# Kernel tuning notes

Measured on AMD Instinct MI355X. Metric: run time of the kernel, lower is better.

## Reference

```python
import jax, jax.numpy as jnp
import numpy as np

V, D, L, H, S, B = 50257, 768, 12, 12, 1024, 2
DH = D // H          # 64
F4 = 4 * D           # 3072
EPS = 1e-5


def _ln(x, g, b):
    m = jnp.mean(x, axis=-1, keepdims=True)
    v = jnp.mean((x - m) ** 2, axis=-1, keepdims=True)
    return (x - m) * jax.lax.rsqrt(v + EPS) * g + b


def setup_inputs() -> dict:
    key = jax.random.key(0)
    ks = jax.random.split(key, 16)
    n = lambda k, shape: jax.random.normal(k, shape, jnp.float32) * 0.02
    return {
        "tokens": jax.random.randint(ks[0], (B, S), 0, V),
        "tok_emb": n(ks[1], (V, D)),
        "pos_emb": n(ks[2], (S, D)),
        "ln1_g": jnp.ones((L, D), jnp.float32), "ln1_b": jnp.zeros((L, D), jnp.float32),
        "wq": n(ks[3], (L, D, D)), "bq": jnp.zeros((L, D), jnp.float32),
        "wk": n(ks[4], (L, D, D)), "bk": jnp.zeros((L, D), jnp.float32),
        "wv": n(ks[5], (L, D, D)), "bv": jnp.zeros((L, D), jnp.float32),
        "wo": n(ks[6], (L, D, D)), "bo": jnp.zeros((L, D), jnp.float32),
        "ln2_g": jnp.ones((L, D), jnp.float32), "ln2_b": jnp.zeros((L, D), jnp.float32),
        "w1": n(ks[7], (L, D, F4)), "b1": jnp.zeros((L, F4), jnp.float32),
        "w2": n(ks[8], (L, F4, D)), "b2": jnp.zeros((L, D), jnp.float32),
        "fn_g": jnp.ones((D,), jnp.float32), "fn_b": jnp.zeros((D,), jnp.float32),
        "head_w": n(ks[9], (D, V)), "head_b": jnp.zeros((V,), jnp.float32),
    }


def reference(tokens, tok_emb, pos_emb, ln1_g, ln1_b, wq, bq, wk, bk, wv, bv,
              wo, bo, ln2_g, ln2_b, w1, b1, w2, b2, fn_g, fn_b, head_w, head_b):
    b_, s_ = tokens.shape
    x = tok_emb[tokens] + pos_emb[:s_]                       # [B,S,D]
    causal = jnp.tril(jnp.ones((s_, s_), bool))              # allow j <= i
    scale = 1.0 / np.sqrt(DH)

    def block(x, p):
        g1, c1, Wq, Bq, Wk, Bk, Wv, Bv_, Wo, Bo, g2, c2, W1, B1, W2, B2 = p
        h = _ln(x, g1, c1)
        q = (h @ Wq + Bq).reshape(b_, s_, H, DH)
        k = (h @ Wk + Bk).reshape(b_, s_, H, DH)
        v = (h @ Wv + Bv_).reshape(b_, s_, H, DH)
        scores = jnp.einsum('bqhd,bkhd->bhqk', q, k) * scale  # [B,H,S,S]
        scores = jnp.where(causal, scores, -jnp.inf)
        attn = jax.nn.softmax(scores, axis=-1)
        o = jnp.einsum('bhqk,bkhd->bqhd', attn, v).reshape(b_, s_, D)
        x = x + (o @ Wo + Bo)
        h2 = _ln(x, g2, c2)
        ff = jax.nn.gelu(h2 @ W1 + B1, approximate=False) @ W2 + B2
        return x + ff, None

    x, _ = jax.lax.scan(block, x, (ln1_g, ln1_b, wq, bq, wk, bk, wv, bv,
                                   wo, bo, ln2_g, ln2_b, w1, b1, w2, b2))
    return _ln(x, fn_g, fn_b) @ head_w + head_b               # [B,S,V]
```

## Files before the change

### kernel.cpp

```cpp
#include <hip/hip_runtime.h>

typedef __bf16 bf16;
typedef bf16 bf16x8 __attribute__((ext_vector_type(8)));
typedef float f32x4 __attribute__((ext_vector_type(4)));

#define SQ  1024
#define DIM 768
#define NH  12
#define NL  12
#define F4  3072
#define NPADV 50304
#define NVOC  50257

__device__ __forceinline__ void async16(bf16* lds, const bf16* g) {
  __builtin_amdgcn_global_load_lds(
      (const __attribute__((address_space(1))) unsigned int*)g,
      (__attribute__((address_space(3))) unsigned int*)lds, 16, 0, 0);
}

__global__ __launch_bounds__(256) void embed_kernel(
    const int* __restrict__ tokens, const float* __restrict__ tok_emb,
    const float* __restrict__ pos_emb, float* __restrict__ x) {
  int row = blockIdx.x;
  int s   = row & (SQ - 1);
  int tok = tokens[row];
  for (int i = threadIdx.x; i < DIM; i += 256)
    x[(size_t)row * DIM + i] = tok_emb[(size_t)tok * DIM + i] + pos_emb[(size_t)s * DIM + i];
}

__global__ __launch_bounds__(256) void ln_kernel(
    const float* __restrict__ x, const float* __restrict__ g,
    const float* __restrict__ b, bf16* __restrict__ out) {
  int row = blockIdx.x;
  const float* xr = x + (size_t)row * DIM;
  int t = threadIdx.x;
  float v0 = xr[t], v1 = xr[t + 256], v2 = xr[t + 512];
  float s  = v0 + v1 + v2;
  float sq = v0 * v0 + v1 * v1 + v2 * v2;
#pragma unroll
  for (int off = 32; off; off >>= 1) {
    s  += __shfl_xor(s, off);
    sq += __shfl_xor(sq, off);
  }
  __shared__ float rs[4], rq[4];
  int wid = t >> 6, lane = t & 63;
  if (lane == 0) { rs[wid] = s; rq[wid] = sq; }
  __syncthreads();
  float S = rs[0] + rs[1] + rs[2] + rs[3];
  float Q = rq[0] + rq[1] + rq[2] + rq[3];
  float mean = S * (1.0f / DIM);
  float var  = Q * (1.0f / DIM) - mean * mean;
  float rstd = rsqrtf(var + 1e-5f);
  bf16* orow = out + (size_t)row * DIM;
  orow[t]       = (bf16)((v0 - mean) * rstd * g[t]       + b[t]);
  orow[t + 256] = (bf16)((v1 - mean) * rstd * g[t + 256] + b[t + 256]);
  orow[t + 512] = (bf16)((v2 - mean) * rstd * g[t + 512] + b[t + 512]);
}

__global__ __launch_bounds__(256) void tconv_kernel(
    const float* __restrict__ src, bf16* __restrict__ dst,
    int K, int N, size_t s_stride, size_t d_stride) {
  __shared__ float tile[32][33];
  const float* s = src + blockIdx.z * s_stride;
  bf16* d = dst + blockIdx.z * d_stride;
  int n0 = blockIdx.x * 32, k0 = blockIdx.y * 32;
  int tx = threadIdx.x & 31, ty = threadIdx.x >> 5;
#pragma unroll
  for (int r = 0; r < 32; r += 8) {
    int n = n0 + tx;
    tile[ty + r][tx] = (n < N) ? s[(size_t)(k0 + ty + r) * N + n] : 0.f;
  }
  __syncthreads();
#pragma unroll
  for (int r = 0; r < 32; r += 8)
    d[(size_t)(n0 + ty + r) * K + k0 + tx] = (bf16)tile[tx][ty + r];
}

__global__ __launch_bounds__(256) void packb_kernel(
    const float* __restrict__ bq, const float* __restrict__ bk,
    const float* __restrict__ bv, float* __restrict__ qkvb) {
  int l = blockIdx.x, t = threadIdx.x;
  for (int i = t; i < DIM; i += 256) {
    qkvb[(size_t)l * 2304 + i]        = bq[(size_t)l * DIM + i];
    qkvb[(size_t)l * 2304 + 768 + i]  = bk[(size_t)l * DIM + i];
    qkvb[(size_t)l * 2304 + 1536 + i] = bv[(size_t)l * DIM + i];
  }
}

template <int BM, int DEPTH, bool GELU_, bool RESID, bool OUTBF, bool NT>
__global__ __launch_bounds__(BM == 128 ? 512 : 256) void gemm_bt(
    const bf16* __restrict__ A, const bf16* __restrict__ BT,
    const float* __restrict__ bias, const float* __restrict__ resid,
    float* __restrict__ outF, bf16* __restrict__ outB,
    int M, int N, int K) {
  constexpr int BK = 64;
  constexpr int WAVES = (BM == 128) ? 8 : 4;
  constexpr int BROW = 128 / WAVES;
  constexpr int NB = BROW / 8;
  constexpr int EPLD = 68;
  constexpr size_t GBYTES = (size_t)DEPTH * (BM + 128) * BK * 2;
  constexpr size_t EBYTES = NT ? (size_t)WAVES * 32 * EPLD * 4 : 0;
  constexpr size_t SBYTES = (EBYTES > GBYTES) ? EBYTES : GBYTES;
  __shared__ __align__(16) char smem[SBYTES];

  const int gx = gridDim.x;
  const int lid = blockIdx.y * gx + blockIdx.x;
  const int q8 = (gx * gridDim.y) >> 3;
  const int work = (lid & 7) * q8 + (lid >> 3);
  const int m0 = (work % gx) * BM, n0 = (work / gx) * 128;

  const int t = threadIdx.x, w = t >> 6, lane = t & 63;
  const int wm = (w >> 1) * 32, wn = (w & 1) * 64;
  const int row16 = lane & 15, kg = lane >> 4;
  const int srow = lane >> 3;
  const int scol = ((lane & 7) ^ srow) * 8;
  f32x4 acc[2][4] = {};

  const bf16* Abase = A  + (size_t)(m0 + w * 16 + srow) * K + scol;
  const bf16* Bbase = BT + (size_t)(n0 + w * BROW + srow) * K + scol;

  auto stage = [&](int buf, int k0) {
    bf16* as = (bf16*)smem + (size_t)buf * BM * BK;
    bf16* bs = (bf16*)smem + (size_t)DEPTH * BM * BK + (size_t)buf * 128 * BK;
#pragma unroll
    for (int i = 0; i < 2; i++)
      async16(as + (w * 16 + i * 8) * BK, Abase + (size_t)(i * 8) * K + k0);
#pragma unroll
    for (int i = 0; i < NB; i++)
      async16(bs + (w * BROW + i * 8) * BK, Bbase + (size_t)(i * 8) * K + k0);
  };

  const int nk = K / BK;
  stage(0, 0);
  if constexpr (DEPTH == 3) stage(1, BK);
  for (int ki = 0; ki < nk; ki++) {
    const int cur = ki % DEPTH;
    const bf16* Ac = (const bf16*)smem + (size_t)cur * BM * BK;
    const bf16* Bc = (const bf16*)smem + (size_t)DEPTH * BM * BK + (size_t)cur * 128 * BK;
    if (ki + DEPTH - 1 < nk) {
      stage((ki + DEPTH - 1) % DEPTH, (ki + DEPTH - 1) * BK);
      if constexpr (DEPTH == 3)      asm volatile("s_waitcnt vmcnt(12)" ::: "memory");
      else if constexpr (BM == 128)  asm volatile("s_waitcnt vmcnt(4)"  ::: "memory");
      else                           asm volatile("s_waitcnt vmcnt(6)"  ::: "memory");
    } else if (DEPTH == 3 && ki + 1 < nk) {
      asm volatile("s_waitcnt vmcnt(6)" ::: "memory");
    } else {
      asm volatile("s_waitcnt vmcnt(0)" ::: "memory");
    }
    __builtin_amdgcn_s_barrier();
    __builtin_amdgcn_sched_barrier(0);
    const int psw = row16 & 7;
#pragma unroll
    for (int kk = 0; kk < 2; kk++) {
      const int pc = ((kk * 4 + kg) ^ psw) * 8;
      bf16x8 af[2], bfv[4];
#pragma unroll
      for (int i = 0; i < 2; i++)
        af[i] = *(const bf16x8*)(&Ac[(wm + i * 16 + row16) * BK + pc]);
#pragma unroll
      for (int j = 0; j < 4; j++)
        bfv[j] = *(const bf16x8*)(&Bc[(wn + j * 16 + row16) * BK + pc]);
#pragma unroll
      for (int i = 0; i < 2; i++)
#pragma unroll
        for (int j = 0; j < 4; j++)
          acc[i][j] = __builtin_amdgcn_mfma_f32_16x16x32_bf16(af[i], bfv[j], acc[i][j], 0, 0, 0);
    }
    if (ki + 1 < nk) {
      __builtin_amdgcn_s_barrier();
      __builtin_amdgcn_sched_barrier(0);
    }
  }

  if constexpr (NT) {
    __syncthreads();
    float* ws = (float*)smem + (size_t)w * 32 * EPLD;
#pragma unroll
    for (int i = 0; i < 2; i++)
#pragma unroll
      for (int j = 0; j < 4; j++) {
        int col = n0 + wn + j * 16 + row16;
        float bi = (col < N) ? bias[col] : 0.f;
#pragma unroll
        for (int r = 0; r < 4; r++)
          ws[(i * 16 + kg * 4 + r) * EPLD + j * 16 + row16] = acc[i][j][r] + bi;
      }
    const int lr = lane >> 4, lc = (lane & 15) * 4;
#pragma unroll
    for (int p = 0; p < 8; p++) {
      int row = m0 + (w >> 1) * 32 + p * 4 + lr;
      int col = n0 + (w & 1) * 64 + lc;
      f32x4 v = *(const f32x4*)&ws[(p * 4 + lr) * EPLD + lc];
      float* dst = outF + (size_t)row * N + col;
      if (col + 3 < N) {
        __builtin_nontemporal_store(v, (f32x4*)dst);
      } else {
#pragma unroll
        for (int e = 0; e < 4; e++)
          if (col + e < N) __builtin_nontemporal_store(v[e], dst + e);
      }
    }
  } else {
#pragma unroll
    for (int i = 0; i < 2; i++)
#pragma unroll
      for (int j = 0; j < 4; j++) {
        int col = n0 + wn + j * 16 + row16;
        if (col < N) {
          float bi = bias[col];
#pragma unroll
          for (int r = 0; r < 4; r++) {
            int row = m0 + wm + i * 16 + kg * 4 + r;
            float val = acc[i][j][r] + bi;
            if constexpr (GELU_) val = 0.5f * val * (1.0f + erff(val * 0.70710678f));
            if constexpr (RESID) val += resid[(size_t)row * N + col];
            if constexpr (OUTBF) outB[(size_t)row * N + col] = (bf16)val;
            else                 outF[(size_t)row * N + col] = val;
          }
        }
      }
  }
}

__global__ __launch_bounds__(512) void fattn_kernel(
    const bf16* __restrict__ qkv, bf16* __restrict__ o) {
  constexpr int LP  = 72;
  constexpr int LPV = 136;
  constexpr int LPP = 136;
  constexpr int LDQ = 2304;
  __shared__ bf16 Ks[128 * LP];
  __shared__ bf16 Vt[64 * LPV];
  __shared__ bf16 Ps[8][16 * LPP];

  const int qt = 7 - (blockIdx.x & 7);
  const int hb = blockIdx.x >> 3;
  const int h  = hb % NH;
  const int b  = hb / NH;
  const int t = threadIdx.x;
  const int w = t >> 6, lane = t & 63;
  const int row16 = lane & 15, kg = lane >> 4;

  const bf16* kbase = qkv + 768  + (size_t)(b * SQ) * LDQ + h * 64;
  const bf16* vbase = qkv + 1536 + (size_t)(b * SQ) * LDQ + h * 64;

  const int wq0  = qt * 128 + w * 16;
  const int qrow = wq0 + row16;
  const bf16* qptr = qkv + (size_t)(b * SQ + qrow) * LDQ + h * 64;
  const bf16x8 qf0 = *(const bf16x8*)(qptr + kg * 8);
  const bf16x8 qf1 = *(const bf16x8*)(qptr + 32 + kg * 8);

  f32x4 oacc[4] = {};
  float mrow[4] = {-1e30f, -1e30f, -1e30f, -1e30f};
  float lrow[4] = {0.f, 0.f, 0.f, 0.f};
  const int myq = wq0 + kg * 4;
  const int ntiles = qt + 1;

  for (int jb0 = 0; jb0 < ntiles; jb0++) {
    const int j0 = jb0 * 128;
    __syncthreads();
#pragma unroll
    for (int it = 0; it < 2; it++) {
      int idx = t + it * 512;
      int key = idx >> 3, d8 = (idx & 7) * 8;
      *(uint4*)(&Ks[key * LP + d8]) =
          *(const uint4*)(kbase + (size_t)(j0 + key) * LDQ + d8);
      bf16x8 vv = *(const bf16x8*)(vbase + (size_t)(j0 + key) * LDQ + d8);
      int kc = key >> 3, kl = key & 7;
#pragma unroll
      for (int e = 0; e < 8; e++) {
        int d = d8 + e;
        Vt[d * LPV + ((kc ^ (d >> 3)) << 3) + kl] = vv[e];
      }
    }
    __syncthreads();

    f32x4 sacc[8];
    __builtin_amdgcn_s_setprio(1);
#pragma unroll
    for (int jb = 0; jb < 8; jb++) {
      bf16x8 kf0 = *(const bf16x8*)(&Ks[(jb * 16 + row16) * LP + kg * 8]);
      bf16x8 kf1 = *(const bf16x8*)(&Ks[(jb * 16 + row16) * LP + 32 + kg * 8]);
      f32x4 sa = {};
      sa = __builtin_amdgcn_mfma_f32_16x16x32_bf16(qf0, kf0, sa, 0, 0, 0);
      sa = __builtin_amdgcn_mfma_f32_16x16x32_bf16(qf1, kf1, sa, 0, 0, 0);
      sacc[jb] = sa;
    }
    __builtin_amdgcn_s_setprio(0);

    constexpr float SC = 0.125f * 1.44269504f;
    if (j0 + 127 > wq0) {
#pragma unroll
      for (int jb = 0; jb < 8; jb++) {
        int keyg = j0 + jb * 16 + row16;
#pragma unroll
        for (int r = 0; r < 4; r++)
          sacc[jb][r] = (keyg <= myq + r) ? sacc[jb][r] * SC : -1e30f;
      }
    } else {
#pragma unroll
      for (int jb = 0; jb < 8; jb++)
#pragma unroll
        for (int r = 0; r < 4; r++)
          sacc[jb][r] *= SC;
    }

    float p[8][4];
#pragma unroll
    for (int r = 0; r < 4; r++) {
      float mx = sacc[0][r];
#pragma unroll
      for (int jb = 1; jb < 8; jb++) mx = fmaxf(mx, sacc[jb][r]);
      mx = fmaxf(mx, __shfl_xor(mx, 1));
      mx = fmaxf(mx, __shfl_xor(mx, 2));
      mx = fmaxf(mx, __shfl_xor(mx, 4));
      mx = fmaxf(mx, __shfl_xor(mx, 8));
      float mn = fmaxf(mrow[r], mx);
      float al = exp2f(mrow[r] - mn);
      mrow[r] = mn;
      float ls = 0.f;
#pragma unroll
      for (int jb = 0; jb < 8; jb++) {
        float pv = exp2f(sacc[jb][r] - mn);
        p[jb][r] = pv;
        ls += pv;
      }
      ls += __shfl_xor(ls, 1);
      ls += __shfl_xor(ls, 2);
      ls += __shfl_xor(ls, 4);
      ls += __shfl_xor(ls, 8);
      lrow[r] = lrow[r] * al + ls;
#pragma unroll
      for (int dt = 0; dt < 4; dt++) oacc[dt][r] *= al;
    }

    bf16* pw = &Ps[w][0];
#pragma unroll
    for (int jb = 0; jb < 8; jb++)
#pragma unroll
      for (int r = 0; r < 4; r++)
        pw[(kg * 4 + r) * LPP + jb * 16 + row16] = (bf16)p[jb][r];

    bf16x8 pf[4];
#pragma unroll
    for (int m = 0; m < 4; m++)
      pf[m] = *(const bf16x8*)(&pw[row16 * LPP + m * 32 + kg * 8]);

    __builtin_amdgcn_s_setprio(1);
#pragma unroll
    for (int dt = 0; dt < 4; dt++) {
      int drow = dt * 16 + row16;
      int sw = drow >> 3;
#pragma unroll
      for (int m = 0; m < 4; m++) {
        bf16x8 vf = *(const bf16x8*)(&Vt[drow * LPV + (((m * 4 + kg) ^ sw) << 3)]);
        oacc[dt] = __builtin_amdgcn_mfma_f32_16x16x32_bf16(pf[m], vf, oacc[dt], 0, 0, 0);
      }
    }
    __builtin_amdgcn_s_setprio(0);
  }

  bf16* obase = o + (size_t)(b * SQ + wq0 + kg * 4) * DIM + h * 64;
#pragma unroll
  for (int r = 0; r < 4; r++) {
    float inv = 1.0f / lrow[r];
#pragma unroll
    for (int dt = 0; dt < 4; dt++)
      obase[(size_t)r * DIM + dt * 16 + row16] = (bf16)(oacc[dt][r] * inv);
  }
}

template <bool GELU_, bool RESID, bool OUTBF>
__global__ __launch_bounds__(256) void gemm_kernel(
    const bf16* __restrict__ A, const float* __restrict__ W,
    const float* __restrict__ bias, const float* __restrict__ resid,
    float* __restrict__ outF, bf16* __restrict__ outB,
    int M, int N, int K) {
  constexpr int BM = 128, BN = 128, BK = 32, LDP = 40;
  __shared__ bf16 As[BM * LDP];
  __shared__ bf16 Bs[BN * LDP];
  int m0 = blockIdx.y * BM;
  int n0 = blockIdx.x * BN;
  int t = threadIdx.x;
  int wid = t >> 6, lane = t & 63;
  int wm = (wid >> 1) * 64, wn = (wid & 1) * 64;
  int row16 = lane & 15, kg = lane >> 4;
  f32x4 acc[4][4] = {};
  bool edge = (n0 + BN > N);

  for (int k0 = 0; k0 < K; k0 += BK) {
#pragma unroll
    for (int r2 = 0; r2 < 2; r2++) {
      int idx = t + r2 * 256;
      int row = idx >> 2, c8 = (idx & 3) * 8;
      uint4 va = *reinterpret_cast<const uint4*>(A + (size_t)(m0 + row) * K + k0 + c8);
      *reinterpret_cast<uint4*>(&As[row * LDP + c8]) = va;
    }
#pragma unroll
    for (int r = 0; r < 8; r++) {
      int idx = t + r * 256;
      int n = idx & 127, kp = idx >> 7;
      int kk = kp * 2;
      float w0 = 0.f, w1 = 0.f;
      if (!edge || (n0 + n) < N) {
        w0 = W[(size_t)(k0 + kk) * N + n0 + n];
        w1 = W[(size_t)(k0 + kk + 1) * N + n0 + n];
      }
      bf16 b0 = (bf16)w0, b1 = (bf16)w1;
      union { bf16 b[2]; unsigned int u; } pk;
      pk.b[0] = b0; pk.b[1] = b1;
      *reinterpret_cast<unsigned int*>(&Bs[n * LDP + kk]) = pk.u;
    }
    __syncthreads();
    bf16x8 af[4], bfv[4];
#pragma unroll
    for (int i = 0; i < 4; i++)
      af[i] = *reinterpret_cast<const bf16x8*>(&As[(wm + i * 16 + row16) * LDP + kg * 8]);
#pragma unroll
    for (int j = 0; j < 4; j++)
      bfv[j] = *reinterpret_cast<const bf16x8*>(&Bs[(wn + j * 16 + row16) * LDP + kg * 8]);
#pragma unroll
    for (int i = 0; i < 4; i++)
#pragma unroll
      for (int j = 0; j < 4; j++)
        acc[i][j] = __builtin_amdgcn_mfma_f32_16x16x32_bf16(af[i], bfv[j], acc[i][j], 0, 0, 0);
    __syncthreads();
  }

  int crow = (lane >> 4) * 4;
  int ccol = lane & 15;
#pragma unroll
  for (int i = 0; i < 4; i++)
#pragma unroll
    for (int j = 0; j < 4; j++) {
      int col = n0 + wn + j * 16 + ccol;
      if (col < N) {
        float bi = bias[col];
#pragma unroll
        for (int r = 0; r < 4; r++) {
          int row = m0 + wm + i * 16 + crow + r;
          float val = acc[i][j][r] + bi;
          if constexpr (GELU_) val = 0.5f * val * (1.0f + erff(val * 0.70710678f));
          if constexpr (RESID) val += resid[(size_t)row * N + col];
          if constexpr (OUTBF) outB[(size_t)row * N + col] = (bf16)val;
          else                 outF[(size_t)row * N + col] = val;
        }
      }
    }
}

__global__ __launch_bounds__(256) void fattn_legacy_kernel(
    const bf16* __restrict__ q, const bf16* __restrict__ k,
    const bf16* __restrict__ v, bf16* __restrict__ o) {
  constexpr int LP = 72;
  __shared__ bf16 Ks[64 * LP];
  __shared__ bf16 Vt[64 * LP];
  __shared__ bf16 Ps[4][16 * LP];
  const int qt = blockIdx.x & 15;
  const int h  = (blockIdx.x >> 4) % NH;
  const int b  = blockIdx.x / (16 * NH);
  const int t = threadIdx.x;
  const int w = t >> 6, lane = t & 63;
  const int row16 = lane & 15, kg = lane >> 4;
  const bf16* kbase = k + (size_t)(b * SQ) * DIM + h * 64;
  const bf16* vbase = v + (size_t)(b * SQ) * DIM + h * 64;
  const int qrow = qt * 64 + w * 16 + row16;
  const bf16* qptr = q + (size_t)(b * SQ + qrow) * DIM + h * 64;
  const bf16x8 qf0 = *(const bf16x8*)(qptr + kg * 8);
  const bf16x8 qf1 = *(const bf16x8*)(qptr + 32 + kg * 8);
  f32x4 oacc[4] = {};
  float mrow[4] = {-1e30f, -1e30f, -1e30f, -1e30f};
  float lrow[4] = {0.f, 0.f, 0.f, 0.f};
  const int myq = qt * 64 + w * 16 + kg * 4;
  for (int jb0 = 0; jb0 <= qt; jb0++) {
    const int j0 = jb0 * 64;
    __syncthreads();
#pragma unroll
    for (int it = 0; it < 2; it++) {
      int idx = t + it * 256;
      int key = idx >> 3, d8 = (idx & 7) * 8;
      *(uint4*)(&Ks[key * LP + d8]) = *(const uint4*)(kbase + (size_t)(j0 + key) * DIM + d8);
    }
#pragma unroll
    for (int it = 0; it < 2; it++) {
      int idx = t + it * 256;
      int key = idx >> 3, d8 = (idx & 7) * 8;
      bf16x8 vv = *(const bf16x8*)(vbase + (size_t)(j0 + key) * DIM + d8);
      int kc = key >> 3, kl = key & 7;
#pragma unroll
      for (int e = 0; e < 8; e++) {
        int d = d8 + e;
        Vt[d * LP + ((kc ^ (d >> 3)) << 3) + kl] = vv[e];
      }
    }
    __syncthreads();
    f32x4 sacc[4];
#pragma unroll
    for (int jb = 0; jb < 4; jb++) {
      bf16x8 kf0 = *(const bf16x8*)(&Ks[(jb * 16 + row16) * LP + kg * 8]);
      bf16x8 kf1 = *(const bf16x8*)(&Ks[(jb * 16 + row16) * LP + 32 + kg * 8]);
      f32x4 sa = {};
      sa = __builtin_amdgcn_mfma_f32_16x16x32_bf16(qf0, kf0, sa, 0, 0, 0);
      sa = __builtin_amdgcn_mfma_f32_16x16x32_bf16(qf1, kf1, sa, 0, 0, 0);
      sacc[jb] = sa;
    }
    constexpr float SC = 0.125f * 1.44269504f;
    if (jb0 == qt) {
#pragma unroll
      for (int jb = 0; jb < 4; jb++) {
        int keyg = j0 + jb * 16 + row16;
#pragma unroll
        for (int r = 0; r < 4; r++)
          sacc[jb][r] = (keyg <= myq + r) ? sacc[jb][r] * SC : -1e30f;
      }
    } else {
#pragma unroll
      for (int jb = 0; jb < 4; jb++)
#pragma unroll
        for (int r = 0; r < 4; r++)
          sacc[jb][r] *= SC;
    }
    float p[4][4];
#pragma unroll
    for (int r = 0; r < 4; r++) {
      float mx = fmaxf(fmaxf(sacc[0][r], sacc[1][r]), fmaxf(sacc[2][r], sacc[3][r]));
      mx = fmaxf(mx, __shfl_xor(mx, 1));
      mx = fmaxf(mx, __shfl_xor(mx, 2));
      mx = fmaxf(mx, __shfl_xor(mx, 4));
      mx = fmaxf(mx, __shfl_xor(mx, 8));
      float mn = fmaxf(mrow[r], mx);
      float al = exp2f(mrow[r] - mn);
      mrow[r] = mn;
      float ls = 0.f;
#pragma unroll
      for (int jb = 0; jb < 4; jb++) {
        float pv = exp2f(sacc[jb][r] - mn);
        p[jb][r] = pv;
        ls += pv;
      }
      ls += __shfl_xor(ls, 1);
      ls += __shfl_xor(ls, 2);
      ls += __shfl_xor(ls, 4);
      ls += __shfl_xor(ls, 8);
      lrow[r] = lrow[r] * al + ls;
#pragma unroll
      for (int dt = 0; dt < 4; dt++) oacc[dt][r] *= al;
    }
    bf16* pw = &Ps[w][0];
#pragma unroll
    for (int jb = 0; jb < 4; jb++)
#pragma unroll
      for (int r = 0; r < 4; r++)
        pw[(kg * 4 + r) * LP + jb * 16 + row16] = (bf16)p[jb][r];
    bf16x8 pf0 = *(const bf16x8*)(&pw[row16 * LP + kg * 8]);
    bf16x8 pf1 = *(const bf16x8*)(&pw[row16 * LP + 32 + kg * 8]);
#pragma unroll
    for (int dt = 0; dt < 4; dt++) {
      int drow = dt * 16 + row16;
      int sw = (drow >> 3) & 7;
      bf16x8 vf0 = *(const bf16x8*)(&Vt[drow * LP + ((kg ^ sw) << 3)]);
      bf16x8 vf1 = *(const bf16x8*)(&Vt[drow * LP + (((4 + kg) ^ sw) << 3)]);
      oacc[dt] = __builtin_amdgcn_mfma_f32_16x16x32_bf16(pf0, vf0, oacc[dt], 0, 0, 0);
      oacc[dt] = __builtin_amdgcn_mfma_f32_16x16x32_bf16(pf1, vf1, oacc[dt], 0, 0, 0);
    }
  }
  bf16* obase = o + (size_t)(b * SQ + qt * 64 + w * 16 + kg * 4) * DIM + h * 64;
#pragma unroll
  for (int r = 0; r < 4; r++) {
    float inv = 1.0f / lrow[r];
#pragma unroll
    for (int dt = 0; dt < 4; dt++)
      obase[(size_t)r * DIM + dt * 16 + row16] = (bf16)(oacc[dt][r] * inv);
  }
}

extern "C" void kernel_launch(void* const* d_in, const int* in_sizes, int n_in,
                              void* d_out, int out_size, void* d_ws, size_t ws_size,
                              hipStream_t stream) {
  const int*   tokens  = (const int*)  d_in[0];
  const float* tok_emb = (const float*)d_in[1];
  const float* pos_emb = (const float*)d_in[2];
  const float* ln1_g   = (const float*)d_in[3];
  const float* ln1_b   = (const float*)d_in[4];
  const float* wq      = (const float*)d_in[5];
  const float* bq      = (const float*)d_in[6];
  const float* wk      = (const float*)d_in[7];
  const float* bk      = (const float*)d_in[8];
  const float* wv      = (const float*)d_in[9];
  const float* bv      = (const float*)d_in[10];
  const float* wo      = (const float*)d_in[11];
  const float* bo      = (const float*)d_in[12];
  const float* ln2_g   = (const float*)d_in[13];
  const float* ln2_b   = (const float*)d_in[14];
  const float* w1      = (const float*)d_in[15];
  const float* b1      = (const float*)d_in[16];
  const float* w2      = (const float*)d_in[17];
  const float* b2      = (const float*)d_in[18];
  const float* fn_g    = (const float*)d_in[19];
  const float* fn_b    = (const float*)d_in[20];
  const float* head_w  = (const float*)d_in[21];
  const float* head_b  = (const float*)d_in[22];
  float* out = (float*)d_out;

  const int ROWS = 2 * SQ;
  char* p = (char*)d_ws;
  float* x   = (float*)p;  p += (size_t)ROWS * DIM * 4;
  bf16*  h   = (bf16*)p;   p += (size_t)ROWS * DIM * 2;
  bf16*  qkv = (bf16*)p;   p += (size_t)ROWS * 2304 * 2;
  bf16*  ao  = (bf16*)p;   p += (size_t)ROWS * DIM * 2;
  bf16*  mid = (bf16*)p;   p += (size_t)ROWS * F4  * 2;
  bf16*  WqkvT = (bf16*)p; p += (size_t)NL * 2304 * DIM * 2;
  bf16*  WoT   = (bf16*)p; p += (size_t)NL * DIM * DIM * 2;
  bf16*  W1T   = (bf16*)p; p += (size_t)NL * F4 * DIM * 2;
  bf16*  W2T   = (bf16*)p; p += (size_t)NL * DIM * F4 * 2;
  bf16*  WhT   = (bf16*)p; p += (size_t)NPADV * DIM * 2;
  float* qkvb  = (float*)p; p += (size_t)NL * 2304 * 4;
  size_t need = (size_t)(p - (char*)d_ws);

  embed_kernel<<<ROWS, 256, 0, stream>>>(tokens, tok_emb, pos_emb, x);

  if (ws_size >= need) {
    {
      dim3 gdd(DIM / 32, DIM / 32, NL);
      size_t ss = (size_t)DIM * DIM, ds = (size_t)2304 * DIM;
      tconv_kernel<<<gdd, 256, 0, stream>>>(wq, WqkvT,                       DIM, DIM, ss, ds);
      tconv_kernel<<<gdd, 256, 0, stream>>>(wk, WqkvT + (size_t)768  * DIM,  DIM, DIM, ss, ds);
      tconv_kernel<<<gdd, 256, 0, stream>>>(wv, WqkvT + (size_t)1536 * DIM,  DIM, DIM, ss, ds);
      tconv_kernel<<<gdd, 256, 0, stream>>>(wo, WoT, DIM, DIM, ss, ss);
      dim3 g1(F4 / 32, DIM / 32, NL);
      tconv_kernel<<<g1, 256, 0, stream>>>(w1, W1T, DIM, F4, (size_t)DIM * F4, (size_t)F4 * DIM);
      dim3 g2(DIM / 32, F4 / 32, NL);
      tconv_kernel<<<g2, 256, 0, stream>>>(w2, W2T, F4, DIM, (size_t)F4 * DIM, (size_t)DIM * F4);
      dim3 gh(NPADV / 32, DIM / 32, 1);
      tconv_kernel<<<gh, 256, 0, stream>>>(head_w, WhT, DIM, NVOC, 0, 0);
      packb_kernel<<<NL, 256, 0, stream>>>(bq, bk, bv, qkvb);
    }

    dim3 gQKV(32, 2304 / 128);
    dim3 gD(32, DIM / 128);
    dim3 gF(32, F4 / 128);
    dim3 gV(16, NPADV / 128);

    for (int l = 0; l < NL; l++) {
      ln_kernel<<<ROWS, 256, 0, stream>>>(x, ln1_g + l * DIM, ln1_b + l * DIM, h);
      gemm_bt<64, 2, false, false, true, false><<<gQKV, 256, 0, stream>>>(
          h, WqkvT + (size_t)l * 2304 * DIM, qkvb + (size_t)l * 2304,
          nullptr, nullptr, qkv, ROWS, 2304, DIM);
      fattn_kernel<<<2 * NH * (SQ / 128), 512, 0, stream>>>(qkv, ao);
      gemm_bt<64, 3, false, true, false, false><<<gD, 256, 0, stream>>>(
          ao, WoT + (size_t)l * DIM * DIM, bo + l * DIM, x, x, nullptr, ROWS, DIM, DIM);
      ln_kernel<<<ROWS, 256, 0, stream>>>(x, ln2_g + l * DIM, ln2_b + l * DIM, h);
      gemm_bt<64, 2, true, false, true, false><<<gF, 256, 0, stream>>>(
          h, W1T + (size_t)l * F4 * DIM, b1 + l * F4, nullptr, nullptr, mid, ROWS, F4, DIM);
      gemm_bt<64, 3, false, true, false, false><<<gD, 256, 0, stream>>>(
          mid, W2T + (size_t)l * DIM * F4, b2 + l * DIM, x, x, nullptr, ROWS, DIM, F4);
    }
    ln_kernel<<<ROWS, 256, 0, stream>>>(x, fn_g, fn_b, h);
    gemm_bt<128, 2, false, false, false, true><<<gV, 512, 0, stream>>>(
        h, WhT, head_b, nullptr, out, nullptr, ROWS, NVOC, DIM);
  } else {
    char* q2 = (char*)d_ws;
    float* xf  = (float*)q2; q2 += (size_t)ROWS * DIM * 4;
    bf16*  hf  = (bf16*)q2;  q2 += (size_t)ROWS * DIM * 2;
    bf16*  qb2 = (bf16*)q2;  q2 += (size_t)ROWS * DIM * 2;
    bf16*  kb2 = (bf16*)q2;  q2 += (size_t)ROWS * DIM * 2;
    bf16*  vb2 = (bf16*)q2;  q2 += (size_t)ROWS * DIM * 2;
    bf16*  ao2 = (bf16*)q2;  q2 += (size_t)ROWS * DIM * 2;
    bf16*  mi2 = (bf16*)q2;  q2 += (size_t)ROWS * F4  * 2;
    dim3 gD(DIM / 128, ROWS / 128);
    dim3 gF(F4 / 128, ROWS / 128);
    dim3 gV((NVOC + 127) / 128, ROWS / 128);
    for (int l = 0; l < NL; l++) {
      size_t wo_off = (size_t)l * DIM * DIM;
      ln_kernel<<<ROWS, 256, 0, stream>>>(xf, ln1_g + l * DIM, ln1_b + l * DIM, hf);
      gemm_kernel<false, false, true><<<gD, 256, 0, stream>>>(
          hf, wq + wo_off, bq + l * DIM, nullptr, nullptr, qb2, ROWS, DIM, DIM);
      gemm_kernel<false, false, true><<<gD, 256, 0, stream>>>(
          hf, wk + wo_off, bk + l * DIM, nullptr, nullptr, kb2, ROWS, DIM, DIM);
      gemm_kernel<false, false, true><<<gD, 256, 0, stream>>>(
          hf, wv + wo_off, bv + l * DIM, nullptr, nullptr, vb2, ROWS, DIM, DIM);
      fattn_legacy_kernel<<<2 * NH * (SQ / 64), 256, 0, stream>>>(qb2, kb2, vb2, ao2);
      gemm_kernel<false, true, false><<<gD, 256, 0, stream>>>(
          ao2, wo + wo_off, bo + l * DIM, xf, xf, nullptr, ROWS, DIM, DIM);
      ln_kernel<<<ROWS, 256, 0, stream>>>(xf, ln2_g + l * DIM, ln2_b + l * DIM, hf);
      gemm_kernel<true, false, true><<<gF, 256, 0, stream>>>(
          hf, w1 + (size_t)l * DIM * F4, b1 + l * F4, nullptr, nullptr, mi2, ROWS, F4, DIM);
      gemm_kernel<false, true, false><<<gD, 256, 0, stream>>>(
          mi2, w2 + (size_t)l * F4 * DIM, b2 + l * DIM, xf, xf, nullptr, ROWS, DIM, F4);
    }
    ln_kernel<<<ROWS, 256, 0, stream>>>(xf, fn_g, fn_b, hf);
    gemm_kernel<false, false, false><<<gV, 256, 0, stream>>>(
        hf, head_w, head_b, nullptr, out, nullptr, ROWS, NVOC, DIM);
  }
}
```

Measured before the change: 1.886 ms.

## Parameterize GEMM wave count, use 4-wave head GEMM, widen transpose stores, drop fallback

The bf16 GEMM template now takes the wave count as a parameter, and the LM-head GEMM runs 4 waves of 256 threads over a 128-row tile, so each wave computes 64x64 instead of 32x64. This gives more MFMA work per LDS fragment load, at the cost of more accumulator registers per thread. The weight transpose/convert kernel now uses 64-wide tiles and writes 16-byte bf16x8 vectors instead of scalar bf16 stores. The legacy fallback path for small workspaces is removed, along with its unused kernels.

```diff
diff --git a/kernel.cpp b/kernel.cpp
--- a/kernel.cpp
+++ b/kernel.cpp
@@ -60,20 +60,24 @@
 __global__ __launch_bounds__(256) void tconv_kernel(
     const float* __restrict__ src, bf16* __restrict__ dst,
     int K, int N, size_t s_stride, size_t d_stride) {
-  __shared__ float tile[32][33];
+  __shared__ float tile[32][65];
   const float* s = src + blockIdx.z * s_stride;
   bf16* d = dst + blockIdx.z * d_stride;
-  int n0 = blockIdx.x * 32, k0 = blockIdx.y * 32;
-  int tx = threadIdx.x & 31, ty = threadIdx.x >> 5;
-#pragma unroll
-  for (int r = 0; r < 32; r += 8) {
-    int n = n0 + tx;
-    tile[ty + r][tx] = (n < N) ? s[(size_t)(k0 + ty + r) * N + n] : 0.f;
+  int n0 = blockIdx.x * 64, k0 = blockIdx.y * 32;
+  int t = threadIdx.x;
+  int nc = t & 63, tk = t >> 6;
+#pragma unroll
+  for (int it = 0; it < 8; it++) {
+    int row = it * 4 + tk;
+    int n = n0 + nc;
+    tile[row][nc] = (n < N) ? s[(size_t)(k0 + row) * N + n] : 0.f;
   }
   __syncthreads();
-#pragma unroll
-  for (int r = 0; r < 32; r += 8)
-    d[(size_t)(n0 + ty + r) * K + k0 + tx] = (bf16)tile[tx][ty + r];
+  int ni = t >> 2, kg = t & 3;
+  bf16x8 v;
+#pragma unroll
+  for (int e = 0; e < 8; e++) v[e] = (bf16)tile[kg * 8 + e][ni];
+  *(bf16x8*)(d + (size_t)(n0 + ni) * K + k0 + kg * 8) = v;
 }
 
 __global__ __launch_bounds__(256) void packb_kernel(
@@ -87,19 +91,24 @@
   }
 }
 
-template <int BM, int DEPTH, bool GELU_, bool RESID, bool OUTBF, bool NT>
-__global__ __launch_bounds__(BM == 128 ? 512 : 256) void gemm_bt(
+template <int BM, int WAVES, int DEPTH, bool GELU_, bool RESID, bool OUTBF, bool NT>
+__global__ __launch_bounds__(WAVES * 64) void gemm_bt(
     const bf16* __restrict__ A, const bf16* __restrict__ BT,
     const float* __restrict__ bias, const float* __restrict__ resid,
     float* __restrict__ outF, bf16* __restrict__ outB,
     int M, int N, int K) {
   constexpr int BK = 64;
-  constexpr int WAVES = (BM == 128) ? 8 : 4;
+  constexpr int WM = 2 * BM / WAVES;
+  constexpr int MI = WM / 16;
+  constexpr int AROW = BM / WAVES;
+  constexpr int NA = AROW / 8;
   constexpr int BROW = 128 / WAVES;
   constexpr int NB = BROW / 8;
+  constexpr int LOADS = NA + NB;
+  constexpr int VMF = (DEPTH - 1) * LOADS;
   constexpr int EPLD = 68;
   constexpr size_t GBYTES = (size_t)DEPTH * (BM + 128) * BK * 2;
-  constexpr size_t EBYTES = NT ? (size_t)WAVES * 32 * EPLD * 4 : 0;
+  constexpr size_t EBYTES = NT ? (size_t)2 * BM * EPLD * 4 : 0;
   constexpr size_t SBYTES = (EBYTES > GBYTES) ? EBYTES : GBYTES;
   __shared__ __align__(16) char smem[SBYTES];
 
@@ -110,21 +119,21 @@
   const int m0 = (work % gx) * BM, n0 = (work / gx) * 128;
 
   const int t = threadIdx.x, w = t >> 6, lane = t & 63;
-  const int wm = (w >> 1) * 32, wn = (w & 1) * 64;
+  const int wm = (w >> 1) * WM, wn = (w & 1) * 64;
   const int row16 = lane & 15, kg = lane >> 4;
   const int srow = lane >> 3;
   const int scol = ((lane & 7) ^ srow) * 8;
-  f32x4 acc[2][4] = {};
-
-  const bf16* Abase = A  + (size_t)(m0 + w * 16 + srow) * K + scol;
+  f32x4 acc[MI][4] = {};
+
+  const bf16* Abase = A  + (size_t)(m0 + w * AROW + srow) * K + scol;
   const bf16* Bbase = BT + (size_t)(n0 + w * BROW + srow) * K + scol;
 
   auto stage = [&](int buf, int k0) {
     bf16* as = (bf16*)smem + (size_t)buf * BM * BK;
     bf16* bs = (bf16*)smem + (size_t)DEPTH * BM * BK + (size_t)buf * 128 * BK;
 #pragma unroll
-    for (int i = 0; i < 2; i++)
-      async16(as + (w * 16 + i * 8) * BK, Abase + (size_t)(i * 8) * K + k0);
+    for (int i = 0; i < NA; i++)
+      async16(as + (w * AROW + i * 8) * BK, Abase + (size_t)(i * 8) * K + k0);
 #pragma unroll
     for (int i = 0; i < NB; i++)
       async16(bs + (w * BROW + i * 8) * BK, Bbase + (size_t)(i * 8) * K + k0);
@@ -139,11 +148,16 @@
     const bf16* Bc = (const bf16*)smem + (size_t)DEPTH * BM * BK + (size_t)cur * 128 * BK;
     if (ki + DEPTH - 1 < nk) {
       stage((ki + DEPTH - 1) % DEPTH, (ki + DEPTH - 1) * BK);
-      if constexpr (DEPTH == 3)      asm volatile("s_waitcnt vmcnt(12)" ::: "memory");
-      else if constexpr (BM == 128)  asm volatile("s_waitcnt vmcnt(4)"  ::: "memory");
-      else                           asm volatile("s_waitcnt vmcnt(6)"  ::: "memory");
-    } else if (DEPTH == 3 && ki + 1 < nk) {
-      asm volatile("s_waitcnt vmcnt(6)" ::: "memory");
+      if constexpr (VMF == 4)       asm volatile("s_waitcnt vmcnt(4)"  ::: "memory");
+      else if constexpr (VMF == 6)  asm volatile("s_waitcnt vmcnt(6)"  ::: "memory");
+      else if constexpr (VMF == 8)  asm volatile("s_waitcnt vmcnt(8)"  ::: "memory");
+      else if constexpr (VMF == 12) asm volatile("s_waitcnt vmcnt(12)" ::: "memory");
+      else if constexpr (VMF == 16) asm volatile("s_waitcnt vmcnt(16)" ::: "memory");
+      else                          asm volatile("s_waitcnt vmcnt(0)"  ::: "memory");
+    } else if (DEPTH == 3 && ki + 2 == nk) {
+      if constexpr (LOADS == 6)     asm volatile("s_waitcnt vmcnt(6)"  ::: "memory");
+      else if constexpr (LOADS == 8) asm volatile("s_waitcnt vmcnt(8)" ::: "memory");
+      else                          asm volatile("s_waitcnt vmcnt(4)"  ::: "memory");
     } else {
       asm volatile("s_waitcnt vmcnt(0)" ::: "memory");
     }
@@ -153,15 +167,15 @@
 #pragma unroll
     for (int kk = 0; kk < 2; kk++) {
       const int pc = ((kk * 4 + kg) ^ psw) * 8;
-      bf16x8 af[2], bfv[4];
-#pragma unroll
-      for (int i = 0; i < 2; i++)
+      bf16x8 af[MI], bfv[4];
+#pragma unroll
+      for (int i = 0; i < MI; i++)
         af[i] = *(const bf16x8*)(&Ac[(wm + i * 16 + row16) * BK + pc]);
 #pragma unroll
       for (int j = 0; j < 4; j++)
         bfv[j] = *(const bf16x8*)(&Bc[(wn + j * 16 + row16) * BK + pc]);
 #pragma unroll
-      for (int i = 0; i < 2; i++)
+      for (int i = 0; i < MI; i++)
 #pragma unroll
         for (int j = 0; j < 4; j++)
           acc[i][j] = __builtin_amdgcn_mfma_f32_16x16x32_bf16(af[i], bfv[j], acc[i][j], 0, 0, 0);
@@ -174,9 +188,9 @@
 
   if constexpr (NT) {
     __syncthreads();
-    float* ws = (float*)smem + (size_t)w * 32 * EPLD;
-#pragma unroll
-    for (int i = 0; i < 2; i++)
+    float* ws = (float*)smem + (size_t)w * WM * EPLD;
+#pragma unroll
+    for (int i = 0; i < MI; i++)
 #pragma unroll
       for (int j = 0; j < 4; j++) {
         int col = n0 + wn + j * 16 + row16;
@@ -187,8 +201,8 @@
       }
     const int lr = lane >> 4, lc = (lane & 15) * 4;
 #pragma unroll
-    for (int p = 0; p < 8; p++) {
-      int row = m0 + (w >> 1) * 32 + p * 4 + lr;
+    for (int p = 0; p < WM / 4; p++) {
+      int row = m0 + (w >> 1) * WM + p * 4 + lr;
       int col = n0 + (w & 1) * 64 + lc;
       f32x4 v = *(const f32x4*)&ws[(p * 4 + lr) * EPLD + lc];
       float* dst = outF + (size_t)row * N + col;
@@ -202,7 +216,7 @@
     }
   } else {
 #pragma unroll
-    for (int i = 0; i < 2; i++)
+    for (int i = 0; i < MI; i++)
 #pragma unroll
       for (int j = 0; j < 4; j++) {
         int col = n0 + wn + j * 16 + row16;
@@ -360,210 +374,6 @@
   }
 
   bf16* obase = o + (size_t)(b * SQ + wq0 + kg * 4) * DIM + h * 64;
-#pragma unroll
-  for (int r = 0; r < 4; r++) {
-    float inv = 1.0f / lrow[r];
-#pragma unroll
-    for (int dt = 0; dt < 4; dt++)
-      obase[(size_t)r * DIM + dt * 16 + row16] = (bf16)(oacc[dt][r] * inv);
-  }
-}
-
-template <bool GELU_, bool RESID, bool OUTBF>
-__global__ __launch_bounds__(256) void gemm_kernel(
-    const bf16* __restrict__ A, const float* __restrict__ W,
-    const float* __restrict__ bias, const float* __restrict__ resid,
-    float* __restrict__ outF, bf16* __restrict__ outB,
-    int M, int N, int K) {
-  constexpr int BM = 128, BN = 128, BK = 32, LDP = 40;
-  __shared__ bf16 As[BM * LDP];
-  __shared__ bf16 Bs[BN * LDP];
-  int m0 = blockIdx.y * BM;
-  int n0 = blockIdx.x * BN;
-  int t = threadIdx.x;
-  int wid = t >> 6, lane = t & 63;
-  int wm = (wid >> 1) * 64, wn = (wid & 1) * 64;
-  int row16 = lane & 15, kg = lane >> 4;
-  f32x4 acc[4][4] = {};
-  bool edge = (n0 + BN > N);
-
-  for (int k0 = 0; k0 < K; k0 += BK) {
-#pragma unroll
-    for (int r2 = 0; r2 < 2; r2++) {
-      int idx = t + r2 * 256;
-      int row = idx >> 2, c8 = (idx & 3) * 8;
-      uint4 va = *reinterpret_cast<const uint4*>(A + (size_t)(m0 + row) * K + k0 + c8);
-      *reinterpret_cast<uint4*>(&As[row * LDP + c8]) = va;
-    }
-#pragma unroll
-    for (int r = 0; r < 8; r++) {
-      int idx = t + r * 256;
-      int n = idx & 127, kp = idx >> 7;
-      int kk = kp * 2;
-      float w0 = 0.f, w1 = 0.f;
-      if (!edge || (n0 + n) < N) {
-        w0 = W[(size_t)(k0 + kk) * N + n0 + n];
-        w1 = W[(size_t)(k0 + kk + 1) * N + n0 + n];
-      }
-      bf16 b0 = (bf16)w0, b1 = (bf16)w1;
-      union { bf16 b[2]; unsigned int u; } pk;
-      pk.b[0] = b0; pk.b[1] = b1;
-      *reinterpret_cast<unsigned int*>(&Bs[n * LDP + kk]) = pk.u;
-    }
-    __syncthreads();
-    bf16x8 af[4], bfv[4];
-#pragma unroll
-    for (int i = 0; i < 4; i++)
-      af[i] = *reinterpret_cast<const bf16x8*>(&As[(wm + i * 16 + row16) * LDP + kg * 8]);
-#pragma unroll
-    for (int j = 0; j < 4; j++)
-      bfv[j] = *reinterpret_cast<const bf16x8*>(&Bs[(wn + j * 16 + row16) * LDP + kg * 8]);
-#pragma unroll
-    for (int i = 0; i < 4; i++)
-#pragma unroll
-      for (int j = 0; j < 4; j++)
-        acc[i][j] = __builtin_amdgcn_mfma_f32_16x16x32_bf16(af[i], bfv[j], acc[i][j], 0, 0, 0);
-    __syncthreads();
-  }
-
-  int crow = (lane >> 4) * 4;
-  int ccol = lane & 15;
-#pragma unroll
-  for (int i = 0; i < 4; i++)
-#pragma unroll
-    for (int j = 0; j < 4; j++) {
-      int col = n0 + wn + j * 16 + ccol;
-      if (col < N) {
-        float bi = bias[col];
-#pragma unroll
-        for (int r = 0; r < 4; r++) {
-          int row = m0 + wm + i * 16 + crow + r;
-          float val = acc[i][j][r] + bi;
-          if constexpr (GELU_) val = 0.5f * val * (1.0f + erff(val * 0.70710678f));
-          if constexpr (RESID) val += resid[(size_t)row * N + col];
-          if constexpr (OUTBF) outB[(size_t)row * N + col] = (bf16)val;
-          else                 outF[(size_t)row * N + col] = val;
-        }
-      }
-    }
-}
-
-__global__ __launch_bounds__(256) void fattn_legacy_kernel(
-    const bf16* __restrict__ q, const bf16* __restrict__ k,
-    const bf16* __restrict__ v, bf16* __restrict__ o) {
-  constexpr int LP = 72;
-  __shared__ bf16 Ks[64 * LP];
-  __shared__ bf16 Vt[64 * LP];
-  __shared__ bf16 Ps[4][16 * LP];
-  const int qt = blockIdx.x & 15;
-  const int h  = (blockIdx.x >> 4) % NH;
-  const int b  = blockIdx.x / (16 * NH);
-  const int t = threadIdx.x;
-  const int w = t >> 6, lane = t & 63;
-  const int row16 = lane & 15, kg = lane >> 4;
-  const bf16* kbase = k + (size_t)(b * SQ) * DIM + h * 64;
-  const bf16* vbase = v + (size_t)(b * SQ) * DIM + h * 64;
-  const int qrow = qt * 64 + w * 16 + row16;
-  const bf16* qptr = q + (size_t)(b * SQ + qrow) * DIM + h * 64;
-  const bf16x8 qf0 = *(const bf16x8*)(qptr + kg * 8);
-  const bf16x8 qf1 = *(const bf16x8*)(qptr + 32 + kg * 8);
-  f32x4 oacc[4] = {};
-  float mrow[4] = {-1e30f, -1e30f, -1e30f, -1e30f};
-  float lrow[4] = {0.f, 0.f, 0.f, 0.f};
-  const int myq = qt * 64 + w * 16 + kg * 4;
-  for (int jb0 = 0; jb0 <= qt; jb0++) {
-    const int j0 = jb0 * 64;
-    __syncthreads();
-#pragma unroll
-    for (int it = 0; it < 2; it++) {
-      int idx = t + it * 256;
-      int key = idx >> 3, d8 = (idx & 7) * 8;
-      *(uint4*)(&Ks[key * LP + d8]) = *(const uint4*)(kbase + (size_t)(j0 + key) * DIM + d8);
-    }
-#pragma unroll
-    for (int it = 0; it < 2; it++) {
-      int idx = t + it * 256;
-      int key = idx >> 3, d8 = (idx & 7) * 8;
-      bf16x8 vv = *(const bf16x8*)(vbase + (size_t)(j0 + key) * DIM + d8);
-      int kc = key >> 3, kl = key & 7;
-#pragma unroll
-      for (int e = 0; e < 8; e++) {
-        int d = d8 + e;
-        Vt[d * LP + ((kc ^ (d >> 3)) << 3) + kl] = vv[e];
-      }
-    }
-    __syncthreads();
-    f32x4 sacc[4];
-#pragma unroll
-    for (int jb = 0; jb < 4; jb++) {
-      bf16x8 kf0 = *(const bf16x8*)(&Ks[(jb * 16 + row16) * LP + kg * 8]);
-      bf16x8 kf1 = *(const bf16x8*)(&Ks[(jb * 16 + row16) * LP + 32 + kg * 8]);
-      f32x4 sa = {};
-      sa = __builtin_amdgcn_mfma_f32_16x16x32_bf16(qf0, kf0, sa, 0, 0, 0);
-      sa = __builtin_amdgcn_mfma_f32_16x16x32_bf16(qf1, kf1, sa, 0, 0, 0);
-      sacc[jb] = sa;
-    }
-    constexpr float SC = 0.125f * 1.44269504f;
-    if (jb0 == qt) {
-#pragma unroll
-      for (int jb = 0; jb < 4; jb++) {
-        int keyg = j0 + jb * 16 + row16;
-#pragma unroll
-        for (int r = 0; r < 4; r++)
-          sacc[jb][r] = (keyg <= myq + r) ? sacc[jb][r] * SC : -1e30f;
-      }
-    } else {
-#pragma unroll
-      for (int jb = 0; jb < 4; jb++)
-#pragma unroll
-        for (int r = 0; r < 4; r++)
-          sacc[jb][r] *= SC;
-    }
-    float p[4][4];
-#pragma unroll
-    for (int r = 0; r < 4; r++) {
-      float mx = fmaxf(fmaxf(sacc[0][r], sacc[1][r]), fmaxf(sacc[2][r], sacc[3][r]));
-      mx = fmaxf(mx, __shfl_xor(mx, 1));
-      mx = fmaxf(mx, __shfl_xor(mx, 2));
-      mx = fmaxf(mx, __shfl_xor(mx, 4));
-      mx = fmaxf(mx, __shfl_xor(mx, 8));
-      float mn = fmaxf(mrow[r], mx);
-      float al = exp2f(mrow[r] - mn);
-      mrow[r] = mn;
-      float ls = 0.f;
-#pragma unroll
-      for (int jb = 0; jb < 4; jb++) {
-        float pv = exp2f(sacc[jb][r] - mn);
-        p[jb][r] = pv;
-        ls += pv;
-      }
-      ls += __shfl_xor(ls, 1);
-      ls += __shfl_xor(ls, 2);
-      ls += __shfl_xor(ls, 4);
-      ls += __shfl_xor(ls, 8);
-      lrow[r] = lrow[r] * al + ls;
-#pragma unroll
-      for (int dt = 0; dt < 4; dt++) oacc[dt][r] *= al;
-    }
-    bf16* pw = &Ps[w][0];
-#pragma unroll
-    for (int jb = 0; jb < 4; jb++)
-#pragma unroll
-      for (int r = 0; r < 4; r++)
-        pw[(kg * 4 + r) * LP + jb * 16 + row16] = (bf16)p[jb][r];
-    bf16x8 pf0 = *(const bf16x8*)(&pw[row16 * LP + kg * 8]);
-    bf16x8 pf1 = *(const bf16x8*)(&pw[row16 * LP + 32 + kg * 8]);
-#pragma unroll
-    for (int dt = 0; dt < 4; dt++) {
-      int drow = dt * 16 + row16;
-      int sw = (drow >> 3) & 7;
-      bf16x8 vf0 = *(const bf16x8*)(&Vt[drow * LP + ((kg ^ sw) << 3)]);
-      bf16x8 vf1 = *(const bf16x8*)(&Vt[drow * LP + (((4 + kg) ^ sw) << 3)]);
-      oacc[dt] = __builtin_amdgcn_mfma_f32_16x16x32_bf16(pf0, vf0, oacc[dt], 0, 0, 0);
-      oacc[dt] = __builtin_amdgcn_mfma_f32_16x16x32_bf16(pf1, vf1, oacc[dt], 0, 0, 0);
-    }
-  }
-  bf16* obase = o + (size_t)(b * SQ + qt * 64 + w * 16 + kg * 4) * DIM + h * 64;
 #pragma unroll
   for (int r = 0; r < 4; r++) {
     float inv = 1.0f / lrow[r];
@@ -615,80 +425,46 @@
   bf16*  WhT   = (bf16*)p; p += (size_t)NPADV * DIM * 2;
   float* qkvb  = (float*)p; p += (size_t)NL * 2304 * 4;
   size_t need = (size_t)(p - (char*)d_ws);
+  (void)need; (void)ws_size;
 
   embed_kernel<<<ROWS, 256, 0, stream>>>(tokens, tok_emb, pos_emb, x);
 
-  if (ws_size >= need) {
-    {
-      dim3 gdd(DIM / 32, DIM / 32, NL);
-      size_t ss = (size_t)DIM * DIM, ds = (size_t)2304 * DIM;
-      tconv_kernel<<<gdd, 256, 0, stream>>>(wq, WqkvT,                       DIM, DIM, ss, ds);
-      tconv_kernel<<<gdd, 256, 0, stream>>>(wk, WqkvT + (size_t)768  * DIM,  DIM, DIM, ss, ds);
-      tconv_kernel<<<gdd, 256, 0, stream>>>(wv, WqkvT + (size_t)1536 * DIM,  DIM, DIM, ss, ds);
-      tconv_kernel<<<gdd, 256, 0, stream>>>(wo, WoT, DIM, DIM, ss, ss);
-      dim3 g1(F4 / 32, DIM / 32, NL);
-      tconv_kernel<<<g1, 256, 0, stream>>>(w1, W1T, DIM, F4, (size_t)DIM * F4, (size_t)F4 * DIM);
-      dim3 g2(DIM / 32, F4 / 32, NL);
-      tconv_kernel<<<g2, 256, 0, stream>>>(w2, W2T, F4, DIM, (size_t)F4 * DIM, (size_t)DIM * F4);
-      dim3 gh(NPADV / 32, DIM / 32, 1);
-      tconv_kernel<<<gh, 256, 0, stream>>>(head_w, WhT, DIM, NVOC, 0, 0);
-      packb_kernel<<<NL, 256, 0, stream>>>(bq, bk, bv, qkvb);
-    }
-
-    dim3 gQKV(32, 2304 / 128);
-    dim3 gD(32, DIM / 128);
-    dim3 gF(32, F4 / 128);
-    dim3 gV(16, NPADV / 128);
-
-    for (int l = 0; l < NL; l++) {
-      ln_kernel<<<ROWS, 256, 0, stream>>>(x, ln1_g + l * DIM, ln1_b + l * DIM, h);
-      gemm_bt<64, 2, false, false, true, false><<<gQKV, 256, 0, stream>>>(
-          h, WqkvT + (size_t)l * 2304 * DIM, qkvb + (size_t)l * 2304,
-          nullptr, nullptr, qkv, ROWS, 2304, DIM);
-      fattn_kernel<<<2 * NH * (SQ / 128), 512, 0, stream>>>(qkv, ao);
-      gemm_bt<64, 3, false, true, false, false><<<gD, 256, 0, stream>>>(
-          ao, WoT + (size_t)l * DIM * DIM, bo + l * DIM, x, x, nullptr, ROWS, DIM, DIM);
-      ln_kernel<<<ROWS, 256, 0, stream>>>(x, ln2_g + l * DIM, ln2_b + l * DIM, h);
-      gemm_bt<64, 2, true, false, true, false><<<gF, 256, 0, stream>>>(
-          h, W1T + (size_t)l * F4 * DIM, b1 + l * F4, nullptr, nullptr, mid, ROWS, F4, DIM);
-      gemm_bt<64, 3, false, true, false, false><<<gD, 256, 0, stream>>>(
-          mid, W2T + (size_t)l * DIM * F4, b2 + l * DIM, x, x, nullptr, ROWS, DIM, F4);
-    }
-    ln_kernel<<<ROWS, 256, 0, stream>>>(x, fn_g, fn_b, h);
-    gemm_bt<128, 2, false, false, false, true><<<gV, 512, 0, stream>>>(
-        h, WhT, head_b, nullptr, out, nullptr, ROWS, NVOC, DIM);
-  } else {
-    char* q2 = (char*)d_ws;
-    float* xf  = (float*)q2; q2 += (size_t)ROWS * DIM * 4;
-    bf16*  hf  = (bf16*)q2;  q2 += (size_t)ROWS * DIM * 2;
-    bf16*  qb2 = (bf16*)q2;  q2 += (size_t)ROWS * DIM * 2;
-    bf16*  kb2 = (bf16*)q2;  q2 += (size_t)ROWS * DIM * 2;
-    bf16*  vb2 = (bf16*)q2;  q2 += (size_t)ROWS * DIM * 2;
-    bf16*  ao2 = (bf16*)q2;  q2 += (size_t)ROWS * DIM * 2;
-    bf16*  mi2 = (bf16*)q2;  q2 += (size_t)ROWS * F4  * 2;
-    dim3 gD(DIM / 128, ROWS / 128);
-    dim3 gF(F4 / 128, ROWS / 128);
-    dim3 gV((NVOC + 127) / 128, ROWS / 128);
-    for (int l = 0; l < NL; l++) {
-      size_t wo_off = (size_t)l * DIM * DIM;
-      ln_kernel<<<ROWS, 256, 0, stream>>>(xf, ln1_g + l * DIM, ln1_b + l * DIM, hf);
-      gemm_kernel<false, false, true><<<gD, 256, 0, stream>>>(
-          hf, wq + wo_off, bq + l * DIM, nullptr, nullptr, qb2, ROWS, DIM, DIM);
-      gemm_kernel<false, false, true><<<gD, 256, 0, stream>>>(
-          hf, wk + wo_off, bk + l * DIM, nullptr, nullptr, kb2, ROWS, DIM, DIM);
-      gemm_kernel<false, false, true><<<gD, 256, 0, stream>>>(
-          hf, wv + wo_off, bv + l * DIM, nullptr, nullptr, vb2, ROWS, DIM, DIM);
-      fattn_legacy_kernel<<<2 * NH * (SQ / 64), 256, 0, stream>>>(qb2, kb2, vb2, ao2);
-      gemm_kernel<false, true, false><<<gD, 256, 0, stream>>>(
-          ao2, wo + wo_off, bo + l * DIM, xf, xf, nullptr, ROWS, DIM, DIM);
-      ln_kernel<<<ROWS, 256, 0, stream>>>(xf, ln2_g + l * DIM, ln2_b + l * DIM, hf);
-      gemm_kernel<true, false, true><<<gF, 256, 0, stream>>>(
-          hf, w1 + (size_t)l * DIM * F4, b1 + l * F4, nullptr, nullptr, mi2, ROWS, F4, DIM);
-      gemm_kernel<false, true, false><<<gD, 256, 0, stream>>>(
-          mi2, w2 + (size_t)l * F4 * DIM, b2 + l * DIM, xf, xf, nullptr, ROWS, DIM, F4);
-    }
-    ln_kernel<<<ROWS, 256, 0, stream>>>(xf, fn_g, fn_b, hf);
-    gemm_kernel<false, false, false><<<gV, 256, 0, stream>>>(
-        hf, head_w, head_b, nullptr, out, nullptr, ROWS, NVOC, DIM);
-  }
-}
+  {
+    dim3 gdd(DIM / 64, DIM / 32, NL);
+    size_t ss = (size_t)DIM * DIM, ds = (size_t)2304 * DIM;
+    tconv_kernel<<<gdd, 256, 0, stream>>>(wq, WqkvT,                       DIM, DIM, ss, ds);
+    tconv_kernel<<<gdd, 256, 0, stream>>>(wk, WqkvT + (size_t)768  * DIM,  DIM, DIM, ss, ds);
+    tconv_kernel<<<gdd, 256, 0, stream>>>(wv, WqkvT + (size_t)1536 * DIM,  DIM, DIM, ss, ds);
+    tconv_kernel<<<gdd, 256, 0, stream>>>(wo, WoT, DIM, DIM, ss, ss);
+    dim3 g1(F4 / 64, DIM / 32, NL);
+    tconv_kernel<<<g1, 256, 0, stream>>>(w1, W1T, DIM, F4, (size_t)DIM * F4, (size_t)F4 * DIM);
+    dim3 g2(DIM / 64, F4 / 32, NL);
+    tconv_kernel<<<g2, 256, 0, stream>>>(w2, W2T, F4, DIM, (size_t)F4 * DIM, (size_t)DIM * F4);
+    dim3 gh(NPADV / 64, DIM / 32, 1);
+    tconv_kernel<<<gh, 256, 0, stream>>>(head_w, WhT, DIM, NVOC, 0, 0);
+    packb_kernel<<<NL, 256, 0, stream>>>(bq, bk, bv, qkvb);
+  }
+
+  dim3 gQKV(32, 2304 / 128);
+  dim3 gD(32, DIM / 128);
+  dim3 gF(32, F4 / 128);
+  dim3 gV(16, NPADV / 128);
+
+  for (int l = 0; l < NL; l++) {
+    ln_kernel<<<ROWS, 256, 0, stream>>>(x, ln1_g + l * DIM, ln1_b + l * DIM, h);
+    gemm_bt<64, 4, 2, false, false, true, false><<<gQKV, 256, 0, stream>>>(
+        h, WqkvT + (size_t)l * 2304 * DIM, qkvb + (size_t)l * 2304,
+        nullptr, nullptr, qkv, ROWS, 2304, DIM);
+    fattn_kernel<<<2 * NH * (SQ / 128), 512, 0, stream>>>(qkv, ao);
+    gemm_bt<64, 4, 3, false, true, false, false><<<gD, 256, 0, stream>>>(
+        ao, WoT + (size_t)l * DIM * DIM, bo + l * DIM, x, x, nullptr, ROWS, DIM, DIM);
+    ln_kernel<<<ROWS, 256, 0, stream>>>(x, ln2_g + l * DIM, ln2_b + l * DIM, h);
+    gemm_bt<64, 4, 2, true, false, true, false><<<gF, 256, 0, stream>>>(
+        h, W1T + (size_t)l * F4 * DIM, b1 + l * F4, nullptr, nullptr, mid, ROWS, F4, DIM);
+    gemm_bt<64, 4, 3, false, true, false, false><<<gD, 256, 0, stream>>>(
+        mid, W2T + (size_t)l * DIM * F4, b2 + l * DIM, x, x, nullptr, ROWS, DIM, F4);
+  }
+  ln_kernel<<<ROWS, 256, 0, stream>>>(x, fn_g, fn_b, h);
+  gemm_bt<128, 4, 2, false, false, false, true><<<gV, 256, 0, stream>>>(
+      h, WhT, head_b, nullptr, out, nullptr, ROWS, NVOC, DIM);
+}
```

Result: slower. 1.933 ms (+2.5%).
